# Performance work log

Hardware: AMD Instinct MI355X
Metric: run time of the kernel (lower is better)

Reference implementation:

```python
import jax, jax.numpy as jnp
import numpy as np

N_NODES = 10000
N_EDGES = 128000


def _edge_conv(x, row, col, edge_attr, w1, b1, w2, b2):
    # gather endpoints, concat edge features, 2-layer MLP per edge
    m = jnp.concatenate([x[row], x[col], edge_attr], axis=1)  # [E, 2*in+edge]
    m = jax.nn.relu(m @ w1 + b1) @ w2 + b2                    # [E, out]
    # scatter-mean onto source nodes (flow='target_to_source' -> aggregate on row)
    n = x.shape[0]
    s = jax.ops.segment_sum(m, row, num_segments=n)
    cnt = jax.ops.segment_sum(jnp.ones((row.shape[0], 1), m.dtype), row, num_segments=n)
    out = s / jnp.maximum(cnt, 1.0)
    return out, m


def setup_inputs() -> dict:
    key = jax.random.key(0)
    ks = jax.random.split(key, 24)
    f = jnp.float32

    def lin(kw, kb, fan_in, fan_out):
        lim = 1.0 / np.sqrt(fan_in)
        w = jax.random.uniform(kw, (fan_in, fan_out), f, -lim, lim)
        b = jax.random.uniform(kb, (fan_out,), f, -lim, lim)
        return w, b

    inp = {}
    inp['x_org'] = jax.random.normal(ks[0], (N_NODES, 256), f)
    inp['x_rot'] = jax.random.normal(ks[1], (N_NODES, 4), f)
    inp['edge_index'] = jax.random.randint(ks[2], (2, N_EDGES), 0, N_NODES, jnp.int64 if jax.config.jax_enable_x64 else jnp.int32)
    inp['edge_attr'] = jax.random.normal(ks[3], (N_EDGES, 640), f)
    inp['edge_rot'] = jax.random.normal(ks[4], (N_EDGES, 4), f)

    # conv1: Linear(2*260+644=1164, 64), Linear(64, 64)
    inp['c1_w1'], inp['c1_b1'] = lin(ks[5], ks[6], 1164, 64)
    inp['c1_w2'], inp['c1_b2'] = lin(ks[7], ks[8], 64, 64)
    # conv2: Linear(2*64+704=832, 64), Linear(64, 64)
    inp['c2_w1'], inp['c2_b1'] = lin(ks[9], ks[10], 832, 64)
    inp['c2_w2'], inp['c2_b2'] = lin(ks[11], ks[12], 64, 64)
    # conv3: Linear(2*128+128=384, 64), Linear(64, 64)
    inp['c3_w1'], inp['c3_b1'] = lin(ks[13], ks[14], 384, 64)
    inp['c3_w2'], inp['c3_b2'] = lin(ks[15], ks[16], 64, 64)
    # conv4: Linear(384, 64), Linear(64, 64)
    inp['c4_w1'], inp['c4_b1'] = lin(ks[17], ks[18], 384, 64)
    inp['c4_w2'], inp['c4_b2'] = lin(ks[19], ks[20], 64, 64)
    # lin1: Linear(64, 4)
    inp['lin1_w'], inp['lin1_b'] = lin(ks[21], ks[22], 64, 4)
    # edge_fc: Linear(64, 32) -> ReLU -> Linear(32, 1)
    k23 = jax.random.split(ks[23], 4)
    inp['efc_w1'], inp['efc_b1'] = lin(k23[0], k23[1], 64, 32)
    inp['efc_w2'], inp['efc_b2'] = lin(k23[2], k23[3], 32, 1)
    return inp


def reference(x_org, x_rot, edge_index, edge_attr, edge_rot,
              c1_w1, c1_b1, c1_w2, c1_b2,
              c2_w1, c2_b1, c2_w2, c2_b2,
              c3_w1, c3_b1, c3_w2, c3_b2,
              c4_w1, c4_b1, c4_w2, c4_b2,
              lin1_w, lin1_b, efc_w1, efc_b1, efc_w2, efc_b2):
    node_feat = jnp.concatenate([x_org, x_rot], axis=1)
    edge_feat = jnp.concatenate([edge_attr, edge_rot], axis=1)
    row, col = edge_index[0], edge_index[1]
    E = edge_index.shape[1]

    x1, edge_x1 = _edge_conv(node_feat, row, col, edge_feat, c1_w1, c1_b1, c1_w2, c1_b2)
    edge_x1 = jax.nn.relu(edge_x1)

    x2, edge_x2 = _edge_conv(x1, row, col, jnp.concatenate([edge_attr, edge_x1], axis=1),
                             c2_w1, c2_b1, c2_w2, c2_b2)
    x2 = jax.nn.relu(x2)
    edge_x2 = jax.nn.relu(edge_x2)

    x3, edge_x3 = _edge_conv(jnp.concatenate([x2, x1], axis=1), row, col,
                             jnp.concatenate([edge_x2, edge_x1], axis=1),
                             c3_w1, c3_b1, c3_w2, c3_b2)
    x3 = jax.nn.relu(x3)
    edge_x3 = jax.nn.relu(edge_x3)

    x4, edge_x4 = _edge_conv(jnp.concatenate([x3, x2], axis=1), row, col,
                             jnp.concatenate([edge_x3, edge_x2], axis=1),
                             c4_w1, c4_b1, c4_w2, c4_b2)
    x4 = jax.nn.relu(x4)

    x = x4 @ lin1_w + lin1_b  # [N, 4]
    h = edge_x4[: E // 2] + edge_x4[E // 2:]
    pred_edge_res = jax.nn.relu(h @ efc_w1 + efc_b1) @ efc_w2 + efc_b2  # [E/2, 1]

    # F.normalize(x, p=2, dim=1)
    x = x / jnp.maximum(jnp.linalg.norm(x, axis=1, keepdims=True), 1e-12)
    return x, pred_edge_res
```

## Files before the change

kernel.cpp:

```cpp
#include <hip/hip_runtime.h>
#include <stdint.h>


#define N_NODES 10000
#define N_EDGES 128000
#define E_HALF  64000

typedef unsigned short u16;

using bf16x8 = __attribute__((ext_vector_type(8))) short;
using f32x4  = __attribute__((ext_vector_type(4))) float;

#define MFMA16(A, B, C) C = __builtin_amdgcn_mfma_f32_16x16x32_bf16(A, B, C, 0, 0, 0)

__device__ __align__(256) float g_acc[N_NODES * 64];
__device__ __align__(256) float g_deg[N_NODES];
__device__ __align__(256) float g_P[N_NODES * 128];
__device__ __align__(256) float g_x1[N_NODES * 64];
__device__ __align__(256) float g_x2[N_NODES * 64];
__device__ __align__(256) float g_x3[N_NODES * 64];
__device__ __align__(256) float g_exA[(size_t)N_EDGES * 64];
__device__ __align__(256) float g_exB[(size_t)N_EDGES * 64];
__device__ __align__(256) u16  g_wpA_hi[11 * 4096];
__device__ __align__(256) u16  g_wpA_lo[11 * 4096];
__device__ __align__(256) u16  g_wp2_hi[4096];
__device__ __align__(256) u16  g_wp2_lo[4096];
__device__ __align__(256) u16  g_wnp_hi[4 * 8192];
__device__ __align__(256) u16  g_wnp_lo[4 * 8192];
__device__ __align__(256) int g_row[N_EDGES];
__device__ __align__(256) int g_col[N_EDGES];
__device__ int g_mode;
__device__ int g_is64;

__device__ __forceinline__ float b2f(u16 u) {
    return __uint_as_float(((unsigned int)u) << 16);
}
__device__ __forceinline__ u16 f2b(float f) {
    unsigned int u = __float_as_uint(f);
    u += 0x7FFFu + ((u >> 16) & 1u);
    return (u16)(u >> 16);
}
__device__ __forceinline__ float ldf(const u16* p)   { return b2f(*p); }
__device__ __forceinline__ float ldf(const float* p) { return *p; }
__device__ __forceinline__ void  stf(u16* p, float v)   { *p = f2b(v); }
__device__ __forceinline__ void  stf(float* p, float v) { *p = v; }

__device__ __forceinline__ float4 load4(const float* p) { return *(const float4*)p; }
__device__ __forceinline__ float4 load4(const u16* p) {
    ushort4 v = *(const ushort4*)p;
    return make_float4(b2f(v.x), b2f(v.y), b2f(v.z), b2f(v.w));
}

template<int KTB>
__device__ __forceinline__ int swz(int b) {
    return b ^ ((b >> 4) & 3) ^ (((b >> KTB) & 1) << 2);
}

__device__ __forceinline__ void split_pack(float4 v, uint2& hi, uint2& lo) {
    unsigned int ux = __float_as_uint(v.x), uy = __float_as_uint(v.y);
    unsigned int uz = __float_as_uint(v.z), uw = __float_as_uint(v.w);
    unsigned int hx = ux & 0xFFFF0000u, hy = uy & 0xFFFF0000u;
    unsigned int hz = uz & 0xFFFF0000u, hw = uw & 0xFFFF0000u;
    hi.x = (hx >> 16) | hy;
    hi.y = (hz >> 16) | hw;
    u16 lx = f2b(v.x - __uint_as_float(hx));
    u16 ly = f2b(v.y - __uint_as_float(hy));
    u16 lz = f2b(v.z - __uint_as_float(hz));
    u16 lw = f2b(v.w - __uint_as_float(hw));
    lo.x = (unsigned int)lx | ((unsigned int)ly << 16);
    lo.y = (unsigned int)lz | ((unsigned int)lw << 16);
}

__global__ void detect_kernel(const void* x_org_v, const int* __restrict__ eidx) {
    const u16* w = (const u16*)x_org_v;
    const int t = threadIdx.x;
    int ok = 0;
    for (int i = t; i < 128; i += 64) {
        u16 v = w[i];
        int ex = (v >> 7) & 0xFF;
        ok += ((ex >= 0x68 && ex <= 0x88) || ((v & 0x7FFFu) == 0)) ? 1 : 0;
    }
    #pragma unroll
    for (int off = 32; off >= 1; off >>= 1) ok += __shfl_xor(ok, off);
    bool allz = true;
    for (int i = t; i < 2048; i += 64) allz = allz && (eidx[2 * i + 1] == 0);
    unsigned long long m = __ballot(allz);
    if (t == 0) {
        g_mode = (ok >= 110) ? 0 : 1;
        g_is64 = (m == ~0ull) ? 1 : 0;
    }
}

__global__ void cvt_idx(const int* __restrict__ eidx) {
    const int e = blockIdx.x * 256 + threadIdx.x;
    if (g_is64) {
        g_row[e] = eidx[2 * e];
        g_col[e] = eidx[2 * (e + N_EDGES)];
    } else {
        g_row[e] = eidx[e];
        g_col[e] = eidx[e + N_EDGES];
    }
}

__global__ void zero_all() {
    const int i = blockIdx.x * 256 + threadIdx.x;
    g_acc[i] = 0.f;
    if (i < N_NODES) g_deg[i] = 0.f;
}

__global__ void deg_kernel() {
    const int e = blockIdx.x * 256 + threadIdx.x;
    if (e < N_EDGES) atomicAdd(&g_deg[g_row[e]], 1.0f);
}

template<typename TW>
__device__ void pack_w_body(const TW* w1, const TW* w2, int we, int ns,
                            int hioff, int nsn) {
    const int idx = blockIdx.x * 256 + threadIdx.x;
    const int t1 = ns * 4096;
    if (idx < t1) {
        const int s = idx >> 12;
        const int rem = idx & 4095;
        const int kt = rem >> 11, ct = (rem >> 9) & 3, l = (rem >> 3) & 63, r = rem & 7;
        const int k = s * 64 + kt * 32 + 4 * (l >> 4) + (r & 3) + 16 * (r >> 2);
        const float v = ldf(w1 + (size_t)(we + k) * 64 + ct * 16 + (l & 15));
        const u16 hh = f2b(v);
        g_wpA_hi[idx] = hh;
        g_wpA_lo[idx] = f2b(v - b2f(hh));
    } else if (idx < t1 + 4096) {
        const int rem = idx - t1;
        const int kt = rem >> 11, ct = (rem >> 9) & 3, l = (rem >> 3) & 63, r = rem & 7;
        const int k = kt * 32 + 4 * (l >> 4) + (r & 3) + 16 * (r >> 2);
        const float v = ldf(w2 + (size_t)k * 64 + ct * 16 + (l & 15));
        const u16 hh = f2b(v);
        g_wp2_hi[rem] = hh;
        g_wp2_lo[rem] = f2b(v - b2f(hh));
    } else if (idx < t1 + 4096 + nsn * 8192) {
        const int rem = idx - t1 - 4096;
        const int s = rem >> 13;
        const int kt = (rem >> 12) & 1, ct = (rem >> 9) & 7, l = (rem >> 3) & 63, r = rem & 7;
        const int k = s * 64 + kt * 32 + 4 * (l >> 4) + (r & 3) + 16 * (r >> 2);
        const int col = ct * 16 + (l & 15);
        const int row = (col < 64) ? k : (hioff + k);
        const float v = ldf(w1 + (size_t)row * 64 + (col & 63));
        const u16 hh = f2b(v);
        g_wnp_hi[rem] = hh;
        g_wnp_lo[rem] = f2b(v - b2f(hh));
    }
}
__global__ void pack_w_k(const void* w1, const void* w2, int we, int ns,
                         int hioff, int nsn) {
    if (g_mode == 0) pack_w_body<u16>((const u16*)w1, (const u16*)w2, we, ns, hioff, nsn);
    else             pack_w_body<float>((const float*)w1, (const float*)w2, we, ns, hioff, nsn);
}

template<typename TA, int NS1, int NS2, bool TAIL>
__device__ void node_mfma_body(u16* smA, float* smrot, float* smwt,
        const TA* A1, const float* A2, const TA* rotsrc, const TA* w1, float* P) {
    constexpr int NS = NS1 + NS2;
    const int t = threadIdx.x;
    const int lane = t & 63, wid = t >> 6;
    const int q = lane >> 4, n = lane & 15;
    const int r0b = blockIdx.x * 64;

    if constexpr (TAIL) {
        if (t < 64) {
            const int rr = min(r0b + t, N_NODES - 1);
            float4 v = load4(rotsrc + (size_t)rr * 4);
            smrot[t * 4 + 0] = v.x; smrot[t * 4 + 1] = v.y;
            smrot[t * 4 + 2] = v.z; smrot[t * 4 + 3] = v.w;
        }
        for (int i = t; i < 512; i += 256) {
            const int j = i >> 7, c = i & 127;
            const int row = (c < 64) ? (256 + j) : (516 + j);
            smwt[i] = ldf(w1 + (size_t)row * 64 + (c & 63));
        }
    }

    f32x4 acc[8];
    #pragma unroll
    for (int ct = 0; ct < 8; ++ct) acc[ct] = (f32x4){0.f, 0.f, 0.f, 0.f};

    const int eb = t >> 4;
    const int cc = t & 15;

    for (int s = 0; s < NS; ++s) {
        #pragma unroll
        for (int p = 0; p < 4; ++p) {
            const int e = p * 16 + eb;
            const int row = min(r0b + e, N_NODES - 1);
            float4 v;
            if constexpr (NS2 > 0)
                v = (s < NS1) ? load4(A1 + (size_t)row * (NS1 * 64) + s * 64 + cc * 4)
                              : load4(A2 + (size_t)row * (NS2 * 64) + (s - NS1) * 64 + cc * 4);
            else
                v = load4(A1 + (size_t)row * (NS1 * 64) + s * 64 + cc * 4);
            uint2 hi, lo; split_pack(v, hi, lo);
            const int blk = ((cc >> 3) * 4 + (e >> 4)) * 64 + (cc & 3) * 16 + (e & 15);
            const int elem = swz<8>(blk) * 8 + ((cc >> 2) & 1) * 4;
            *(uint2*)&smA[elem]        = hi;
            *(uint2*)&smA[elem + 4096] = lo;
        }
        __syncthreads();
        const u16* wph = g_wnp_hi + s * 8192;
        const u16* wpl = g_wnp_lo + s * 8192;
        #pragma unroll
        for (int kt = 0; kt < 2; ++kt) {
            const int ad = swz<8>((kt * 4 + wid) * 64 + lane) * 8;
            bf16x8 ah = *(const bf16x8*)&smA[ad];
            bf16x8 al = *(const bf16x8*)&smA[ad + 4096];
            #pragma unroll
            for (int ct = 0; ct < 8; ++ct) {
                bf16x8 bh = *(const bf16x8*)&wph[(kt * 8 + ct) * 512 + lane * 8];
                bf16x8 bl = *(const bf16x8*)&wpl[(kt * 8 + ct) * 512 + lane * 8];
                MFMA16(ah, bh, acc[ct]);
                MFMA16(al, bh, acc[ct]);
                MFMA16(ah, bl, acc[ct]);
            }
        }
        __syncthreads();
    }

    #pragma unroll
    for (int ct = 0; ct < 8; ++ct) {
        #pragma unroll
        for (int i = 0; i < 4; ++i) {
            const int rl = wid * 16 + 4 * q + i;
            const int row = r0b + rl;
            const int col = ct * 16 + n;
            float v = acc[ct][i];
            if constexpr (TAIL)
                v += smrot[rl * 4 + 0] * smwt[0 * 128 + col]
                   + smrot[rl * 4 + 1] * smwt[1 * 128 + col]
                   + smrot[rl * 4 + 2] * smwt[2 * 128 + col]
                   + smrot[rl * 4 + 3] * smwt[3 * 128 + col];
            if (row < N_NODES) P[(size_t)row * 128 + col] = v;
        }
    }
}

template<int NS1, bool TAIL>
__global__ void __launch_bounds__(256) node_mfma_in(
        const void* A1, const void* rotsrc, const void* w1, float* __restrict__ P) {
    __shared__ u16 smA[8192];
    __shared__ float smrot[256], smwt[512];
    if (g_mode == 0)
        node_mfma_body<u16, NS1, 0, TAIL>(smA, smrot, smwt, (const u16*)A1,
            nullptr, (const u16*)rotsrc, (const u16*)w1, P);
    else
        node_mfma_body<float, NS1, 0, TAIL>(smA, smrot, smwt, (const float*)A1,
            nullptr, (const float*)rotsrc, (const float*)w1, P);
}

template<int NS1, int NS2>
__global__ void __launch_bounds__(256) node_mfma_ws(
        const float* A1, const float* A2, float* __restrict__ P) {
    __shared__ u16 smA[8192];
    __shared__ float smrot[256], smwt[512];
    node_mfma_body<float, NS1, NS2, false>(smA, smrot, smwt, A1, A2,
        (const float*)nullptr, (const float*)nullptr, P);
}

template<typename TA, typename TW, int NSA, int DB, bool RELU_OUT>
__device__ __forceinline__ void edge_mfma_body(
        u16* smA, int* srow, int* scol, float* b1s, float* b2s,
        float* rot, float* wtl,
        const TA* efa, const float* efb, const TA* rotsrc,
        const TW* w1, const TW* b1v, const TW* b2v, float* eout, int we) {
    constexpr int NS_TOT = NSA + (DB == 64 ? 1 : 0);
    const int t = threadIdx.x;
    const int lane = t & 63, wid = t >> 6;
    const int q = lane >> 4, n = lane & 15;
    const int e0 = blockIdx.x * 128;

    if (t < 128) srow[t] = g_row[e0 + t];
    else         scol[t - 128] = g_col[e0 + t - 128];
    if (t >= 128 && t < 192) b1s[t - 128] = ldf(b1v + (t - 128));
    if (t >= 192)            b2s[t - 192] = ldf(b2v + (t - 192));
    if constexpr (DB == 4) {
        if (t < 128) {
            float4 r4 = load4(rotsrc + (size_t)(e0 + t) * 4);
            rot[t * 4 + 0] = r4.x; rot[t * 4 + 1] = r4.y;
            rot[t * 4 + 2] = r4.z; rot[t * 4 + 3] = r4.w;
        }
        wtl[t] = ldf(w1 + (size_t)(we + NSA * 64 + (t >> 6)) * 64 + (t & 63));
    }

    f32x4 acc[2][4];
    #pragma unroll
    for (int a_ = 0; a_ < 2; ++a_)
        #pragma unroll
        for (int b_ = 0; b_ < 4; ++b_)
            acc[a_][b_] = (f32x4){0.f, 0.f, 0.f, 0.f};

    const int eb = t >> 4;
    const int cc = t & 15;

    for (int s = 0; s < NS_TOT; ++s) {
        #pragma unroll
        for (int p = 0; p < 8; ++p) {
            const int e = p * 16 + eb;
            float4 v;
            if (s < NSA) v = load4(efa + (size_t)(e0 + e) * (NSA * 64) + s * 64 + cc * 4);
            else         v = load4(efb + (size_t)(e0 + e) * 64 + cc * 4);
            uint2 hi, lo; split_pack(v, hi, lo);
            const int blk = ((cc >> 3) * 8 + (e >> 4)) * 64 + (cc & 3) * 16 + (e & 15);
            const int elem = swz<9>(blk) * 8 + ((cc >> 2) & 1) * 4;
            *(uint2*)&smA[elem]        = hi;
            *(uint2*)&smA[elem + 8192] = lo;
        }
        __syncthreads();
        const u16* wph = g_wpA_hi + s * 4096;
        const u16* wpl = g_wpA_lo + s * 4096;
        #pragma unroll
        for (int kt = 0; kt < 2; ++kt) {
            const int b0 = (kt * 8 + wid * 2 + 0) * 64 + lane;
            const int b1 = (kt * 8 + wid * 2 + 1) * 64 + lane;
            const int r0 = swz<9>(b0) * 8;
            const int r1 = swz<9>(b1) * 8;
            bf16x8 ah0 = *(const bf16x8*)&smA[r0];
            bf16x8 ah1 = *(const bf16x8*)&smA[r1];
            bf16x8 al0 = *(const bf16x8*)&smA[r0 + 8192];
            bf16x8 al1 = *(const bf16x8*)&smA[r1 + 8192];
            #pragma unroll
            for (int ct = 0; ct < 4; ++ct) {
                bf16x8 bh = *(const bf16x8*)&wph[(kt * 4 + ct) * 512 + lane * 8];
                bf16x8 bl = *(const bf16x8*)&wpl[(kt * 4 + ct) * 512 + lane * 8];
                MFMA16(ah0, bh, acc[0][ct]);
                MFMA16(ah1, bh, acc[1][ct]);
                MFMA16(al0, bh, acc[0][ct]);
                MFMA16(al1, bh, acc[1][ct]);
                MFMA16(ah0, bl, acc[0][ct]);
                MFMA16(ah1, bl, acc[1][ct]);
            }
        }
        __syncthreads();
    }

    #pragma unroll
    for (int rt = 0; rt < 2; ++rt) {
        #pragma unroll
        for (int ct = 0; ct < 4; ++ct) {
            #pragma unroll
            for (int i = 0; i < 4; ++i) {
                const int rl = wid * 32 + rt * 16 + 4 * q + i;
                const int col = ct * 16 + n;
                float v = acc[rt][ct][i] + b1s[col]
                        + g_P[(size_t)srow[rl] * 128 + col]
                        + g_P[(size_t)scol[rl] * 128 + 64 + col];
                if constexpr (DB == 4) {
                    v += rot[rl * 4 + 0] * wtl[0 * 64 + col]
                       + rot[rl * 4 + 1] * wtl[1 * 64 + col]
                       + rot[rl * 4 + 2] * wtl[2 * 64 + col]
                       + rot[rl * 4 + 3] * wtl[3 * 64 + col];
                }
                v = fmaxf(v, 0.f);
                unsigned int hb = __float_as_uint(v) & 0xFFFF0000u;
                const u16 hh = (u16)(hb >> 16);
                const u16 hl = f2b(v - __uint_as_float(hb));
                const int off = wid * 4096
                              + (((ct >> 1) * 2 + rt) * 64 + (n >> 2) * 16 + 4 * q + i) * 8
                              + (ct & 1) * 4 + (n & 3);
                smA[off]        = hh;
                smA[off + 2048] = hl;
            }
        }
    }

    f32x4 oacc[2][4];
    #pragma unroll
    for (int rt = 0; rt < 2; ++rt)
        #pragma unroll
        for (int ct = 0; ct < 4; ++ct) {
            const float bb = b2s[ct * 16 + n];
            oacc[rt][ct] = (f32x4){bb, bb, bb, bb};
        }
    #pragma unroll
    for (int kt = 0; kt < 2; ++kt) {
        const int r0 = wid * 4096 + ((kt * 2 + 0) * 64 + lane) * 8;
        const int r1 = wid * 4096 + ((kt * 2 + 1) * 64 + lane) * 8;
        bf16x8 ah0 = *(const bf16x8*)&smA[r0];
        bf16x8 ah1 = *(const bf16x8*)&smA[r1];
        bf16x8 al0 = *(const bf16x8*)&smA[r0 + 2048];
        bf16x8 al1 = *(const bf16x8*)&smA[r1 + 2048];
        #pragma unroll
        for (int ct = 0; ct < 4; ++ct) {
            bf16x8 bh = *(const bf16x8*)&g_wp2_hi[(kt * 4 + ct) * 512 + lane * 8];
            bf16x8 bl = *(const bf16x8*)&g_wp2_lo[(kt * 4 + ct) * 512 + lane * 8];
            MFMA16(ah0, bh, oacc[0][ct]);
            MFMA16(ah1, bh, oacc[1][ct]);
            MFMA16(al0, bh, oacc[0][ct]);
            MFMA16(al1, bh, oacc[1][ct]);
            MFMA16(ah0, bl, oacc[0][ct]);
            MFMA16(ah1, bl, oacc[1][ct]);
        }
    }

    #pragma unroll
    for (int rt = 0; rt < 2; ++rt) {
        #pragma unroll
        for (int ct = 0; ct < 4; ++ct) {
            #pragma unroll
            for (int i = 0; i < 4; ++i) {
                const int rl = wid * 32 + rt * 16 + 4 * q + i;
                const int col = ct * 16 + n;
                const float v = oacc[rt][ct][i];
                atomicAdd(&g_acc[(size_t)srow[rl] * 64 + col], v);
                eout[(size_t)(e0 + rl) * 64 + col] = RELU_OUT ? fmaxf(v, 0.f) : v;
            }
        }
    }
}

template<int NSA, int DB, bool RELU_OUT>
__global__ void __launch_bounds__(256, 4) edge_mfma_in(
        const void* efa, const float* efb, const void* rotsrc,
        const void* w1, const void* b1, const void* b2, float* eout, int we) {
    __shared__ u16 smA[16384];
    __shared__ int srow[128], scol[128];
    __shared__ float b1s[64], b2s[64], rot[512], wtl[256];
    if (g_mode == 0)
        edge_mfma_body<u16, u16, NSA, DB, RELU_OUT>(smA, srow, scol, b1s, b2s, rot, wtl,
            (const u16*)efa, efb, (const u16*)rotsrc,
            (const u16*)w1, (const u16*)b1, (const u16*)b2, eout, we);
    else
        edge_mfma_body<float, float, NSA, DB, RELU_OUT>(smA, srow, scol, b1s, b2s, rot, wtl,
            (const float*)efa, efb, (const float*)rotsrc,
            (const float*)w1, (const float*)b1, (const float*)b2, eout, we);
}

template<int NSA, int DB, bool RELU_OUT>
__global__ void __launch_bounds__(256, 4) edge_mfma_ws(
        const float* efa, const float* efb,
        const void* w1, const void* b1, const void* b2, float* eout, int we) {
    __shared__ u16 smA[16384];
    __shared__ int srow[128], scol[128];
    __shared__ float b1s[64], b2s[64], rot[512], wtl[256];
    if (g_mode == 0)
        edge_mfma_body<float, u16, NSA, DB, RELU_OUT>(smA, srow, scol, b1s, b2s, rot, wtl,
            efa, efb, (const float*)nullptr,
            (const u16*)w1, (const u16*)b1, (const u16*)b2, eout, we);
    else
        edge_mfma_body<float, float, NSA, DB, RELU_OUT>(smA, srow, scol, b1s, b2s, rot, wtl,
            efa, efb, (const float*)nullptr,
            (const float*)w1, (const float*)b1, (const float*)b2, eout, we);
}

template<bool RELU>
__global__ void finalize_k(float* __restrict__ dst) {
    const int idx = blockIdx.x * 256 + threadIdx.x;
    float v = g_acc[idx] / fmaxf(g_deg[idx >> 6], 1.0f);
    g_acc[idx] = 0.f;
    if (RELU) v = fmaxf(v, 0.f);
    dst[idx] = v;
}

template<typename T>
__device__ void final_node_body(const T* w, const T* b, T* out) {
    const int t = threadIdx.x;
    const int lane = t & 63;
    const int n = blockIdx.x * 4 + (t >> 6);
    float inv = 1.0f / fmaxf(g_deg[n], 1.0f);
    float x4 = fmaxf(g_acc[(size_t)n * 64 + lane] * inv, 0.0f);
    float r[4];
    #pragma unroll
    for (int j = 0; j < 4; ++j) {
        float v = x4 * ldf(w + lane * 4 + j);
        #pragma unroll
        for (int off = 32; off >= 1; off >>= 1) v += __shfl_xor(v, off);
        r[j] = v + ldf(b + j);
    }
    float nrm = sqrtf(r[0]*r[0] + r[1]*r[1] + r[2]*r[2] + r[3]*r[3]);
    float dn = fmaxf(nrm, 1e-12f);
    if (lane < 4) stf(out + n * 4 + lane, r[lane] / dn);
}
__global__ void final_node(const void* w, const void* b, void* out) {
    if (g_mode == 0) final_node_body<u16>((const u16*)w, (const u16*)b, (u16*)out);
    else             final_node_body<float>((const float*)w, (const float*)b, (float*)out);
}

template<typename T>
__device__ void edge_head_body(const float* ex4, const T* w1, const T* b1,
                               const T* w2, const T* b2, T* out) {
    __shared__ float lw1[2048];
    __shared__ float lw2[32];
    const int t = threadIdx.x;
    for (int i = t; i < 2048; i += 256) lw1[i] = ldf(w1 + i);
    if (t < 32) lw2[t] = ldf(w2 + t);
    __syncthreads();
    const int e = blockIdx.x * 256 + t;
    float a[32];
    #pragma unroll
    for (int j = 0; j < 32; ++j) a[j] = ldf(b1 + j);
    const float* p0 = ex4 + (size_t)e * 64;
    const float* p1 = ex4 + (size_t)(e + E_HALF) * 64;
    for (int c = 0; c < 64; ++c) {
        float h = p0[c] + p1[c];
        #pragma unroll
        for (int j = 0; j < 32; ++j) a[j] += h * lw1[c * 32 + j];
    }
    float s = ldf(b2);
    #pragma unroll
    for (int j = 0; j < 32; ++j) s += fmaxf(a[j], 0.f) * lw2[j];
    stf(out + e, s);
}
__global__ void __launch_bounds__(256) edge_head(const float* ex4,
        const void* w1, const void* b1, const void* w2, const void* b2,
        void* out) {
    if (g_mode == 0)
        edge_head_body<u16>(ex4, (const u16*)w1, (const u16*)b1,
                            (const u16*)w2, (const u16*)b2, (u16*)out + 40000);
    else
        edge_head_body<float>(ex4, (const float*)w1, (const float*)b1,
                              (const float*)w2, (const float*)b2, (float*)out + 40000);
}

__global__ void sentinel_fill(unsigned int* out, int n_words) {
    int i = blockIdx.x * 256 + threadIdx.x;
    if (i < n_words) out[i] = 0x44794479u;
}

static void* sym_addr(const void* symbol) {
    void* p = nullptr;
    (void)hipGetSymbolAddress(&p, symbol);
    return p;
}

extern "C" void kernel_launch(void* const* d_in, const int* in_sizes, int n_in,
                              void* d_out, int out_size, void* d_ws, size_t ws_size,
                              hipStream_t stream) {
    (void)d_ws; (void)ws_size;
    bool ok = (n_in == 27) && (out_size == 104000)
           && (in_sizes[0] == 2560000) && (in_sizes[2] == 256000)
           && (in_sizes[3] == 81920000) && (in_sizes[5] == 74496)
           && (in_sizes[21] == 256) && (in_sizes[25] == 32);
    if (!ok) {
        sentinel_fill<<<204, 256, 0, stream>>>((unsigned int*)d_out, 52000);
        return;
    }
    const void* x_org     = d_in[0];
    const void* x_rot     = d_in[1];
    const int*  eidx      = (const int*)d_in[2];
    const void* edge_attr = d_in[3];
    const void* edge_rot  = d_in[4];

    float* P   = (float*)sym_addr(HIP_SYMBOL(g_P));
    float* x1  = (float*)sym_addr(HIP_SYMBOL(g_x1));
    float* x2  = (float*)sym_addr(HIP_SYMBOL(g_x2));
    float* x3  = (float*)sym_addr(HIP_SYMBOL(g_x3));
    float* exA = (float*)sym_addr(HIP_SYMBOL(g_exA));
    float* exB = (float*)sym_addr(HIP_SYMBOL(g_exB));

    detect_kernel<<<1, 64, 0, stream>>>(x_org, eidx);
    cvt_idx<<<500, 256, 0, stream>>>(eidx);
    zero_all<<<2500, 256, 0, stream>>>();
    deg_kernel<<<500, 256, 0, stream>>>();

    pack_w_k<<<304, 256, 0, stream>>>(d_in[5], d_in[7], 520, 10, 260, 4);
    node_mfma_in<4, true><<<157, 256, 0, stream>>>(x_org, x_rot, d_in[5], P);
    edge_mfma_in<10, 4, true><<<1000, 256, 0, stream>>>(
        edge_attr, nullptr, edge_rot, d_in[5], d_in[6], d_in[8], exA, 520);
    finalize_k<false><<<2500, 256, 0, stream>>>(x1);

    pack_w_k<<<224, 256, 0, stream>>>(d_in[9], d_in[11], 128, 11, 64, 1);
    node_mfma_ws<1, 0><<<157, 256, 0, stream>>>(x1, nullptr, P);
    edge_mfma_in<10, 64, true><<<1000, 256, 0, stream>>>(
        edge_attr, exA, nullptr, d_in[9], d_in[10], d_in[12], exB, 128);
    finalize_k<true><<<2500, 256, 0, stream>>>(x2);

    pack_w_k<<<112, 256, 0, stream>>>(d_in[13], d_in[15], 256, 2, 128, 2);
    node_mfma_ws<1, 1><<<157, 256, 0, stream>>>(x2, x1, P);
    edge_mfma_ws<1, 64, true><<<1000, 256, 0, stream>>>(
        exB, exA, d_in[13], d_in[14], d_in[16], exA, 256);
    finalize_k<true><<<2500, 256, 0, stream>>>(x3);

    pack_w_k<<<112, 256, 0, stream>>>(d_in[17], d_in[19], 256, 2, 128, 2);
    node_mfma_ws<1, 1><<<157, 256, 0, stream>>>(x3, x2, P);
    edge_mfma_ws<1, 64, false><<<1000, 256, 0, stream>>>(
        exA, exB, d_in[17], d_in[18], d_in[20], exB, 256);

    final_node<<<2500, 256, 0, stream>>>(d_in[21], d_in[22], d_out);
    edge_head<<<250, 256, 0, stream>>>(exB, d_in[23], d_in[24], d_in[25], d_in[26],
                                       d_out);
}
```

Baseline: 922.8 us.

## Fuse edge_attr projections for conv1/conv2 and pass edge features as MFMA fragments

The conv1 edge kernel now multiplies edge_attr by a combined 128-column weight holding both the conv1 and conv2 edge_attr rows. The conv2 contribution is saved to a Q2 buffer, so conv2 no longer re-reads the 640-wide edge_attr. Intermediate edge outputs are written as pre-split bf16 hi/lo MFMA fragment tiles, and later layers load them straight into registers instead of repacking fp32 through shared memory. This removes a second full pass over the large edge_attr tensor and the repacking cost. In exchange it adds a Q2 round trip and more accumulator registers in conv1, with occupancy lowered to 3 blocks per unit.

```diff
diff --git a/kernel.cpp b/kernel.cpp
--- a/kernel.cpp
+++ b/kernel.cpp
@@ -5,6 +5,7 @@
 #define N_NODES 10000
 #define N_EDGES 128000
 #define E_HALF  64000
+#define NBLK    1000
 
 typedef unsigned short u16;
 
@@ -19,14 +20,18 @@
 __device__ __align__(256) float g_x1[N_NODES * 64];
 __device__ __align__(256) float g_x2[N_NODES * 64];
 __device__ __align__(256) float g_x3[N_NODES * 64];
-__device__ __align__(256) float g_exA[(size_t)N_EDGES * 64];
-__device__ __align__(256) float g_exB[(size_t)N_EDGES * 64];
-__device__ __align__(256) u16  g_wpA_hi[11 * 4096];
-__device__ __align__(256) u16  g_wpA_lo[11 * 4096];
+__device__ __align__(256) u16  g_fragA[(size_t)NBLK * 16384];
+__device__ __align__(256) u16  g_fragB[(size_t)NBLK * 16384];
+__device__ __align__(256) float g_Q2 [(size_t)N_EDGES * 64];
+__device__ __align__(256) float g_ex4[(size_t)N_EDGES * 64];
+__device__ __align__(256) u16  g_wpA_hi[2 * 4096];
+__device__ __align__(256) u16  g_wpA_lo[2 * 4096];
 __device__ __align__(256) u16  g_wp2_hi[4096];
 __device__ __align__(256) u16  g_wp2_lo[4096];
 __device__ __align__(256) u16  g_wnp_hi[4 * 8192];
 __device__ __align__(256) u16  g_wnp_lo[4 * 8192];
+__device__ __align__(256) u16  g_wpC_hi[10 * 8192];
+__device__ __align__(256) u16  g_wpC_lo[10 * 8192];
 __device__ __align__(256) int g_row[N_EDGES];
 __device__ __align__(256) int g_col[N_EDGES];
 __device__ int g_mode;
@@ -114,20 +119,22 @@
 }
 
 template<typename TW>
-__device__ void pack_w_body(const TW* w1, const TW* w2, int we, int ns,
-                            int hioff, int nsn) {
+__device__ void pack_w_body(const TW* w1a, const TW* w2, const TW* w1b,
+                            int we, int ns, int hioff, int nsn, int nsc) {
     const int idx = blockIdx.x * 256 + threadIdx.x;
     const int t1 = ns * 4096;
+    const int t2 = t1 + 4096;
+    const int t3 = t2 + nsn * 8192;
     if (idx < t1) {
         const int s = idx >> 12;
         const int rem = idx & 4095;
         const int kt = rem >> 11, ct = (rem >> 9) & 3, l = (rem >> 3) & 63, r = rem & 7;
         const int k = s * 64 + kt * 32 + 4 * (l >> 4) + (r & 3) + 16 * (r >> 2);
-        const float v = ldf(w1 + (size_t)(we + k) * 64 + ct * 16 + (l & 15));
+        const float v = ldf(w1a + (size_t)(we + k) * 64 + ct * 16 + (l & 15));
         const u16 hh = f2b(v);
         g_wpA_hi[idx] = hh;
         g_wpA_lo[idx] = f2b(v - b2f(hh));
-    } else if (idx < t1 + 4096) {
+    } else if (idx < t2) {
         const int rem = idx - t1;
         const int kt = rem >> 11, ct = (rem >> 9) & 3, l = (rem >> 3) & 63, r = rem & 7;
         const int k = kt * 32 + 4 * (l >> 4) + (r & 3) + 16 * (r >> 2);
@@ -135,23 +142,39 @@
         const u16 hh = f2b(v);
         g_wp2_hi[rem] = hh;
         g_wp2_lo[rem] = f2b(v - b2f(hh));
-    } else if (idx < t1 + 4096 + nsn * 8192) {
-        const int rem = idx - t1 - 4096;
+    } else if (idx < t3) {
+        const int rem = idx - t2;
         const int s = rem >> 13;
         const int kt = (rem >> 12) & 1, ct = (rem >> 9) & 7, l = (rem >> 3) & 63, r = rem & 7;
         const int k = s * 64 + kt * 32 + 4 * (l >> 4) + (r & 3) + 16 * (r >> 2);
         const int col = ct * 16 + (l & 15);
         const int row = (col < 64) ? k : (hioff + k);
-        const float v = ldf(w1 + (size_t)row * 64 + (col & 63));
+        const float v = ldf(w1a + (size_t)row * 64 + (col & 63));
         const u16 hh = f2b(v);
         g_wnp_hi[rem] = hh;
         g_wnp_lo[rem] = f2b(v - b2f(hh));
-    }
-}
-__global__ void pack_w_k(const void* w1, const void* w2, int we, int ns,
-                         int hioff, int nsn) {
-    if (g_mode == 0) pack_w_body<u16>((const u16*)w1, (const u16*)w2, we, ns, hioff, nsn);
-    else             pack_w_body<float>((const float*)w1, (const float*)w2, we, ns, hioff, nsn);
+    } else if (idx < t3 + nsc * 8192) {
+        const int rem = idx - t3;
+        const int s = rem >> 13;
+        const int kt = (rem >> 12) & 1, ct = (rem >> 9) & 7, l = (rem >> 3) & 63, r = rem & 7;
+        const int k = s * 64 + kt * 32 + 4 * (l >> 4) + (r & 3) + 16 * (r >> 2);
+        const int col = ct * 16 + (l & 15);
+        float v;
+        if (col < 64) v = ldf(w1a + (size_t)(520 + k) * 64 + col);
+        else          v = ldf(w1b + (size_t)(128 + k) * 64 + (col - 64));
+        const u16 hh = f2b(v);
+        g_wpC_hi[rem] = hh;
+        g_wpC_lo[rem] = f2b(v - b2f(hh));
+    }
+}
+__global__ void pack_w_k(const void* w1a, const void* w2, const void* w1b,
+                         int we, int ns, int hioff, int nsn, int nsc) {
+    if (g_mode == 0)
+        pack_w_body<u16>((const u16*)w1a, (const u16*)w2, (const u16*)w1b,
+                         we, ns, hioff, nsn, nsc);
+    else
+        pack_w_body<float>((const float*)w1a, (const float*)w2, (const float*)w1b,
+                         we, ns, hioff, nsn, nsc);
 }
 
 template<typename TA, int NS1, int NS2, bool TAIL>
@@ -261,13 +284,44 @@
         (const float*)nullptr, (const float*)nullptr, P);
 }
 
-template<typename TA, typename TW, int NSA, int DB, bool RELU_OUT>
-__device__ __forceinline__ void edge_mfma_body(
-        u16* smA, int* srow, int* scol, float* b1s, float* b2s,
-        float* rot, float* wtl,
-        const TA* efa, const float* efb, const TA* rotsrc,
-        const TW* w1, const TW* b1v, const TW* b2v, float* eout, int we) {
-    constexpr int NS_TOT = NSA + (DB == 64 ? 1 : 0);
+__device__ __forceinline__ void frag_store_o(u16* smA, int wid, int lane,
+        const f32x4 (&oacc)[2][4], u16* Fdst, int blkid) {
+    const int q = lane >> 4, n = lane & 15;
+    #pragma unroll
+    for (int rt = 0; rt < 2; ++rt)
+        #pragma unroll
+        for (int ct = 0; ct < 4; ++ct)
+            #pragma unroll
+            for (int i = 0; i < 4; ++i) {
+                float v = fmaxf(oacc[rt][ct][i], 0.f);
+                unsigned int hb = __float_as_uint(v) & 0xFFFF0000u;
+                const u16 hh = (u16)(hb >> 16);
+                const u16 hl = f2b(v - __uint_as_float(hb));
+                const int off = wid * 4096
+                              + (((ct >> 1) * 2 + rt) * 64 + (n >> 2) * 16 + 4 * q + i) * 8
+                              + (ct & 1) * 4 + (n & 3);
+                smA[off]        = hh;
+                smA[off + 2048] = hl;
+            }
+    #pragma unroll
+    for (int kt = 0; kt < 2; ++kt)
+        #pragma unroll
+        for (int rtl = 0; rtl < 2; ++rtl) {
+            const int src = wid * 4096 + ((kt * 2 + rtl) * 64 + lane) * 8;
+            bf16x8 h8 = *(const bf16x8*)&smA[src];
+            bf16x8 l8 = *(const bf16x8*)&smA[src + 2048];
+            const size_t gb = (size_t)blkid * 16384
+                            + (size_t)(kt * 8 + wid * 2 + rtl) * 512 + lane * 8;
+            *(bf16x8*)&Fdst[gb]        = h8;
+            *(bf16x8*)&Fdst[gb + 8192] = l8;
+        }
+}
+
+template<typename TA, typename TW>
+__device__ void edge_c1_body(u16* smA, int* srow, int* scol,
+        float* b1s, float* b2s, float* rot, float* wtl,
+        const TA* efa, const TA* rotsrc,
+        const TW* w1, const TW* b1v, const TW* b2v) {
     const int t = threadIdx.x;
     const int lane = t & 63, wid = t >> 6;
     const int q = lane >> 4, n = lane & 15;
@@ -277,32 +331,28 @@
     else         scol[t - 128] = g_col[e0 + t - 128];
     if (t >= 128 && t < 192) b1s[t - 128] = ldf(b1v + (t - 128));
     if (t >= 192)            b2s[t - 192] = ldf(b2v + (t - 192));
-    if constexpr (DB == 4) {
-        if (t < 128) {
-            float4 r4 = load4(rotsrc + (size_t)(e0 + t) * 4);
-            rot[t * 4 + 0] = r4.x; rot[t * 4 + 1] = r4.y;
-            rot[t * 4 + 2] = r4.z; rot[t * 4 + 3] = r4.w;
-        }
-        wtl[t] = ldf(w1 + (size_t)(we + NSA * 64 + (t >> 6)) * 64 + (t & 63));
-    }
-
-    f32x4 acc[2][4];
+    if (t < 128) {
+        float4 r4 = load4(rotsrc + (size_t)(e0 + t) * 4);
+        rot[t * 4 + 0] = r4.x; rot[t * 4 + 1] = r4.y;
+        rot[t * 4 + 2] = r4.z; rot[t * 4 + 3] = r4.w;
+    }
+    wtl[t] = ldf(w1 + (size_t)(1160 + (t >> 6)) * 64 + (t & 63));
+
+    f32x4 acc[2][8];
     #pragma unroll
     for (int a_ = 0; a_ < 2; ++a_)
         #pragma unroll
-        for (int b_ = 0; b_ < 4; ++b_)
+        for (int b_ = 0; b_ < 8; ++b_)
             acc[a_][b_] = (f32x4){0.f, 0.f, 0.f, 0.f};
 
     const int eb = t >> 4;
     const int cc = t & 15;
 
-    for (int s = 0; s < NS_TOT; ++s) {
+    for (int s = 0; s < 10; ++s) {
         #pragma unroll
         for (int p = 0; p < 8; ++p) {
             const int e = p * 16 + eb;
-            float4 v;
-            if (s < NSA) v = load4(efa + (size_t)(e0 + e) * (NSA * 64) + s * 64 + cc * 4);
-            else         v = load4(efb + (size_t)(e0 + e) * 64 + cc * 4);
+            float4 v = load4(efa + (size_t)(e0 + e) * 640 + s * 64 + cc * 4);
             uint2 hi, lo; split_pack(v, hi, lo);
             const int blk = ((cc >> 3) * 8 + (e >> 4)) * 64 + (cc & 3) * 16 + (e & 15);
             const int elem = swz<9>(blk) * 8 + ((cc >> 2) & 1) * 4;
@@ -310,18 +360,163 @@
             *(uint2*)&smA[elem + 8192] = lo;
         }
         __syncthreads();
-        const u16* wph = g_wpA_hi + s * 4096;
-        const u16* wpl = g_wpA_lo + s * 4096;
+        const u16* wph = g_wpC_hi + s * 8192;
+        const u16* wpl = g_wpC_lo + s * 8192;
         #pragma unroll
         for (int kt = 0; kt < 2; ++kt) {
             const int b0 = (kt * 8 + wid * 2 + 0) * 64 + lane;
-            const int b1 = (kt * 8 + wid * 2 + 1) * 64 + lane;
+            const int b1i = (kt * 8 + wid * 2 + 1) * 64 + lane;
             const int r0 = swz<9>(b0) * 8;
-            const int r1 = swz<9>(b1) * 8;
+            const int r1 = swz<9>(b1i) * 8;
             bf16x8 ah0 = *(const bf16x8*)&smA[r0];
             bf16x8 ah1 = *(const bf16x8*)&smA[r1];
             bf16x8 al0 = *(const bf16x8*)&smA[r0 + 8192];
             bf16x8 al1 = *(const bf16x8*)&smA[r1 + 8192];
+            #pragma unroll
+            for (int ct = 0; ct < 8; ++ct) {
+                bf16x8 bh = *(const bf16x8*)&wph[(kt * 8 + ct) * 512 + lane * 8];
+                bf16x8 bl = *(const bf16x8*)&wpl[(kt * 8 + ct) * 512 + lane * 8];
+                MFMA16(ah0, bh, acc[0][ct]);
+                MFMA16(ah1, bh, acc[1][ct]);
+                MFMA16(al0, bh, acc[0][ct]);
+                MFMA16(al1, bh, acc[1][ct]);
+                MFMA16(ah0, bl, acc[0][ct]);
+                MFMA16(ah1, bl, acc[1][ct]);
+            }
+        }
+        __syncthreads();
+    }
+
+    #pragma unroll
+    for (int rt = 0; rt < 2; ++rt)
+        #pragma unroll
+        for (int c2 = 0; c2 < 4; ++c2)
+            #pragma unroll
+            for (int i = 0; i < 4; ++i) {
+                const int rl = wid * 32 + rt * 16 + 4 * q + i;
+                g_Q2[(size_t)(e0 + rl) * 64 + c2 * 16 + n] = acc[rt][4 + c2][i];
+            }
+
+    #pragma unroll
+    for (int rt = 0; rt < 2; ++rt)
+        #pragma unroll
+        for (int ct = 0; ct < 4; ++ct)
+            #pragma unroll
+            for (int i = 0; i < 4; ++i) {
+                const int rl = wid * 32 + rt * 16 + 4 * q + i;
+                const int col = ct * 16 + n;
+                float v = acc[rt][ct][i] + b1s[col]
+                        + g_P[(size_t)srow[rl] * 128 + col]
+                        + g_P[(size_t)scol[rl] * 128 + 64 + col]
+                        + rot[rl * 4 + 0] * wtl[0 * 64 + col]
+                        + rot[rl * 4 + 1] * wtl[1 * 64 + col]
+                        + rot[rl * 4 + 2] * wtl[2 * 64 + col]
+                        + rot[rl * 4 + 3] * wtl[3 * 64 + col];
+                v = fmaxf(v, 0.f);
+                unsigned int hb = __float_as_uint(v) & 0xFFFF0000u;
+                const u16 hh = (u16)(hb >> 16);
+                const u16 hl = f2b(v - __uint_as_float(hb));
+                const int off = wid * 4096
+                              + (((ct >> 1) * 2 + rt) * 64 + (n >> 2) * 16 + 4 * q + i) * 8
+                              + (ct & 1) * 4 + (n & 3);
+                smA[off]        = hh;
+                smA[off + 2048] = hl;
+            }
+
+    f32x4 oacc[2][4];
+    #pragma unroll
+    for (int rt = 0; rt < 2; ++rt)
+        #pragma unroll
+        for (int ct = 0; ct < 4; ++ct) {
+            const float bb = b2s[ct * 16 + n];
+            oacc[rt][ct] = (f32x4){bb, bb, bb, bb};
+        }
+    #pragma unroll
+    for (int kt = 0; kt < 2; ++kt) {
+        const int r0 = wid * 4096 + ((kt * 2 + 0) * 64 + lane) * 8;
+        const int r1 = wid * 4096 + ((kt * 2 + 1) * 64 + lane) * 8;
+        bf16x8 ah0 = *(const bf16x8*)&smA[r0];
+        bf16x8 ah1 = *(const bf16x8*)&smA[r1];
+        bf16x8 al0 = *(const bf16x8*)&smA[r0 + 2048];
+        bf16x8 al1 = *(const bf16x8*)&smA[r1 + 2048];
+        #pragma unroll
+        for (int ct = 0; ct < 4; ++ct) {
+            bf16x8 bh = *(const bf16x8*)&g_wp2_hi[(kt * 4 + ct) * 512 + lane * 8];
+            bf16x8 bl = *(const bf16x8*)&g_wp2_lo[(kt * 4 + ct) * 512 + lane * 8];
+            MFMA16(ah0, bh, oacc[0][ct]);
+            MFMA16(ah1, bh, oacc[1][ct]);
+            MFMA16(al0, bh, oacc[0][ct]);
+            MFMA16(al1, bh, oacc[1][ct]);
+            MFMA16(ah0, bl, oacc[0][ct]);
+            MFMA16(ah1, bl, oacc[1][ct]);
+        }
+    }
+
+    #pragma unroll
+    for (int rt = 0; rt < 2; ++rt)
+        #pragma unroll
+        for (int ct = 0; ct < 4; ++ct)
+            #pragma unroll
+            for (int i = 0; i < 4; ++i) {
+                const int rl = wid * 32 + rt * 16 + 4 * q + i;
+                atomicAdd(&g_acc[(size_t)srow[rl] * 64 + ct * 16 + n], oacc[rt][ct][i]);
+            }
+    frag_store_o(smA, wid, lane, oacc, g_fragA, blockIdx.x);
+}
+
+__global__ void __launch_bounds__(256, 3) edge_c1(
+        const void* efa, const void* rotsrc,
+        const void* w1, const void* b1, const void* b2) {
+    __shared__ u16 smA[16384];
+    __shared__ int srow[128], scol[128];
+    __shared__ float b1s[64], b2s[64], rot[512], wtl[256];
+    if (g_mode == 0)
+        edge_c1_body<u16, u16>(smA, srow, scol, b1s, b2s, rot, wtl,
+            (const u16*)efa, (const u16*)rotsrc,
+            (const u16*)w1, (const u16*)b1, (const u16*)b2);
+    else
+        edge_c1_body<float, float>(smA, srow, scol, b1s, b2s, rot, wtl,
+            (const float*)efa, (const float*)rotsrc,
+            (const float*)w1, (const float*)b1, (const float*)b2);
+}
+
+template<typename TW, int NSF, bool HASQ2, bool FRAG_OUT>
+__device__ void edge_lite_body(u16* smA, int* srow, int* scol,
+        float* b1s, float* b2s,
+        const u16* f0, const u16* f1,
+        const TW* b1v, const TW* b2v, u16* Ffrag, float* fout) {
+    const int t = threadIdx.x;
+    const int lane = t & 63, wid = t >> 6;
+    const int q = lane >> 4, n = lane & 15;
+    const int e0 = blockIdx.x * 128;
+    const size_t blkb = (size_t)blockIdx.x * 16384;
+
+    if (t < 128) srow[t] = g_row[e0 + t];
+    else         scol[t - 128] = g_col[e0 + t - 128];
+    if (t >= 128 && t < 192) b1s[t - 128] = ldf(b1v + (t - 128));
+    if (t >= 192)            b2s[t - 192] = ldf(b2v + (t - 192));
+    __syncthreads();
+
+    f32x4 acc[2][4];
+    #pragma unroll
+    for (int a_ = 0; a_ < 2; ++a_)
+        #pragma unroll
+        for (int b_ = 0; b_ < 4; ++b_)
+            acc[a_][b_] = (f32x4){0.f, 0.f, 0.f, 0.f};
+
+    #pragma unroll
+    for (int s = 0; s < NSF; ++s) {
+        const u16* fs = (s == 0) ? f0 : f1;
+        const u16* wph = g_wpA_hi + s * 4096;
+        const u16* wpl = g_wpA_lo + s * 4096;
+        #pragma unroll
+        for (int kt = 0; kt < 2; ++kt) {
+            const size_t ba0 = blkb + (size_t)(kt * 8 + wid * 2 + 0) * 512 + lane * 8;
+            const size_t ba1 = blkb + (size_t)(kt * 8 + wid * 2 + 1) * 512 + lane * 8;
+            bf16x8 ah0 = *(const bf16x8*)&fs[ba0];
+            bf16x8 al0 = *(const bf16x8*)&fs[ba0 + 8192];
+            bf16x8 ah1 = *(const bf16x8*)&fs[ba1];
+            bf16x8 al1 = *(const bf16x8*)&fs[ba1 + 8192];
             #pragma unroll
             for (int ct = 0; ct < 4; ++ct) {
                 bf16x8 bh = *(const bf16x8*)&wph[(kt * 4 + ct) * 512 + lane * 8];
@@ -334,13 +529,12 @@
                 MFMA16(ah1, bl, acc[1][ct]);
             }
         }
-        __syncthreads();
-    }
-
-    #pragma unroll
-    for (int rt = 0; rt < 2; ++rt) {
-        #pragma unroll
-        for (int ct = 0; ct < 4; ++ct) {
+    }
+
+    #pragma unroll
+    for (int rt = 0; rt < 2; ++rt)
+        #pragma unroll
+        for (int ct = 0; ct < 4; ++ct)
             #pragma unroll
             for (int i = 0; i < 4; ++i) {
                 const int rl = wid * 32 + rt * 16 + 4 * q + i;
@@ -348,12 +542,8 @@
                 float v = acc[rt][ct][i] + b1s[col]
                         + g_P[(size_t)srow[rl] * 128 + col]
                         + g_P[(size_t)scol[rl] * 128 + 64 + col];
-                if constexpr (DB == 4) {
-                    v += rot[rl * 4 + 0] * wtl[0 * 64 + col]
-                       + rot[rl * 4 + 1] * wtl[1 * 64 + col]
-                       + rot[rl * 4 + 2] * wtl[2 * 64 + col]
-                       + rot[rl * 4 + 3] * wtl[3 * 64 + col];
-                }
+                if constexpr (HASQ2)
+                    v += g_Q2[(size_t)(e0 + rl) * 64 + col];
                 v = fmaxf(v, 0.f);
                 unsigned int hb = __float_as_uint(v) & 0xFFFF0000u;
                 const u16 hh = (u16)(hb >> 16);
@@ -364,8 +554,6 @@
                 smA[off]        = hh;
                 smA[off + 2048] = hl;
             }
-        }
-    }
 
     f32x4 oacc[2][4];
     #pragma unroll
@@ -397,53 +585,35 @@
     }
 
     #pragma unroll
-    for (int rt = 0; rt < 2; ++rt) {
-        #pragma unroll
-        for (int ct = 0; ct < 4; ++ct) {
+    for (int rt = 0; rt < 2; ++rt)
+        #pragma unroll
+        for (int ct = 0; ct < 4; ++ct)
             #pragma unroll
             for (int i = 0; i < 4; ++i) {
                 const int rl = wid * 32 + rt * 16 + 4 * q + i;
                 const int col = ct * 16 + n;
                 const float v = oacc[rt][ct][i];
                 atomicAdd(&g_acc[(size_t)srow[rl] * 64 + col], v);
-                eout[(size_t)(e0 + rl) * 64 + col] = RELU_OUT ? fmaxf(v, 0.f) : v;
-            }
-        }
-    }
-}
-
-template<int NSA, int DB, bool RELU_OUT>
-__global__ void __launch_bounds__(256, 4) edge_mfma_in(
-        const void* efa, const float* efb, const void* rotsrc,
-        const void* w1, const void* b1, const void* b2, float* eout, int we) {
+                if constexpr (!FRAG_OUT)
+                    fout[(size_t)(e0 + rl) * 64 + col] = v;
+            }
+    if constexpr (FRAG_OUT)
+        frag_store_o(smA, wid, lane, oacc, Ffrag, blockIdx.x);
+}
+
+template<int NSF, bool HASQ2, bool FRAG_OUT>
+__global__ void __launch_bounds__(256, 4) edge_lite(
+        const u16* f0, const u16* f1, const void* b1, const void* b2,
+        u16* Ffrag, float* fout) {
     __shared__ u16 smA[16384];
     __shared__ int srow[128], scol[128];
-    __shared__ float b1s[64], b2s[64], rot[512], wtl[256];
+    __shared__ float b1s[64], b2s[64];
     if (g_mode == 0)
-        edge_mfma_body<u16, u16, NSA, DB, RELU_OUT>(smA, srow, scol, b1s, b2s, rot, wtl,
-            (const u16*)efa, efb, (const u16*)rotsrc,
-            (const u16*)w1, (const u16*)b1, (const u16*)b2, eout, we);
+        edge_lite_body<u16, NSF, HASQ2, FRAG_OUT>(smA, srow, scol, b1s, b2s,
+            f0, f1, (const u16*)b1, (const u16*)b2, Ffrag, fout);
     else
-        edge_mfma_body<float, float, NSA, DB, RELU_OUT>(smA, srow, scol, b1s, b2s, rot, wtl,
-            (const float*)efa, efb, (const float*)rotsrc,
-            (const float*)w1, (const float*)b1, (const float*)b2, eout, we);
-}
-
-template<int NSA, int DB, bool RELU_OUT>
-__global__ void __launch_bounds__(256, 4) edge_mfma_ws(
-        const float* efa, const float* efb,
-        const void* w1, const void* b1, const void* b2, float* eout, int we) {
-    __shared__ u16 smA[16384];
-    __shared__ int srow[128], scol[128];
-    __shared__ float b1s[64], b2s[64], rot[512], wtl[256];
-    if (g_mode == 0)
-        edge_mfma_body<float, u16, NSA, DB, RELU_OUT>(smA, srow, scol, b1s, b2s, rot, wtl,
-            efa, efb, (const float*)nullptr,
-            (const u16*)w1, (const u16*)b1, (const u16*)b2, eout, we);
-    else
-        edge_mfma_body<float, float, NSA, DB, RELU_OUT>(smA, srow, scol, b1s, b2s, rot, wtl,
-            efa, efb, (const float*)nullptr,
-            (const float*)w1, (const float*)b1, (const float*)b2, eout, we);
+        edge_lite_body<float, NSF, HASQ2, FRAG_OUT>(smA, srow, scol, b1s, b2s,
+            f0, f1, (const float*)b1, (const float*)b2, Ffrag, fout);
 }
 
 template<bool RELU>
@@ -548,38 +718,38 @@
     float* x1  = (float*)sym_addr(HIP_SYMBOL(g_x1));
     float* x2  = (float*)sym_addr(HIP_SYMBOL(g_x2));
     float* x3  = (float*)sym_addr(HIP_SYMBOL(g_x3));
-    float* exA = (float*)sym_addr(HIP_SYMBOL(g_exA));
-    float* exB = (float*)sym_addr(HIP_SYMBOL(g_exB));
+    u16*   fA  = (u16*)sym_addr(HIP_SYMBOL(g_fragA));
+    u16*   fB  = (u16*)sym_addr(HIP_SYMBOL(g_fragB));
+    float* ex4 = (float*)sym_addr(HIP_SYMBOL(g_ex4));
 
     detect_kernel<<<1, 64, 0, stream>>>(x_org, eidx);
     cvt_idx<<<500, 256, 0, stream>>>(eidx);
     zero_all<<<2500, 256, 0, stream>>>();
     deg_kernel<<<500, 256, 0, stream>>>();
 
-    pack_w_k<<<304, 256, 0, stream>>>(d_in[5], d_in[7], 520, 10, 260, 4);
+    pack_w_k<<<464, 256, 0, stream>>>(d_in[5], d_in[7], d_in[9], 0, 0, 260, 4, 10);
     node_mfma_in<4, true><<<157, 256, 0, stream>>>(x_org, x_rot, d_in[5], P);
-    edge_mfma_in<10, 4, true><<<1000, 256, 0, stream>>>(
-        edge_attr, nullptr, edge_rot, d_in[5], d_in[6], d_in[8], exA, 520);
+    edge_c1<<<NBLK, 256, 0, stream>>>(edge_attr, edge_rot, d_in[5], d_in[6], d_in[8]);
     finalize_k<false><<<2500, 256, 0, stream>>>(x1);
 
-    pack_w_k<<<224, 256, 0, stream>>>(d_in[9], d_in[11], 128, 11, 64, 1);
+    pack_w_k<<<64, 256, 0, stream>>>(d_in[9], d_in[11], d_in[9], 768, 1, 64, 1, 0);
     node_mfma_ws<1, 0><<<157, 256, 0, stream>>>(x1, nullptr, P);
-    edge_mfma_in<10, 64, true><<<1000, 256, 0, stream>>>(
-        edge_attr, exA, nullptr, d_in[9], d_in[10], d_in[12], exB, 128);
+    edge_lite<1, true, true><<<NBLK, 256, 0, stream>>>(
+        fA, nullptr, d_in[10], d_in[12], fB, nullptr);
     finalize_k<true><<<2500, 256, 0, stream>>>(x2);
 
-    pack_w_k<<<112, 256, 0, stream>>>(d_in[13], d_in[15], 256, 2, 128, 2);
+    pack_w_k<<<112, 256, 0, stream>>>(d_in[13], d_in[15], d_in[13], 256, 2, 128, 2, 0);
     node_mfma_ws<1, 1><<<157, 256, 0, stream>>>(x2, x1, P);
-    edge_mfma_ws<1, 64, true><<<1000, 256, 0, stream>>>(
-        exB, exA, d_in[13], d_in[14], d_in[16], exA, 256);
+    edge_lite<2, false, true><<<NBLK, 256, 0, stream>>>(
+        fB, fA, d_in[14], d_in[16], fA, nullptr);
     finalize_k<true><<<2500, 256, 0, stream>>>(x3);
 
-    pack_w_k<<<112, 256, 0, stream>>>(d_in[17], d_in[19], 256, 2, 128, 2);
+    pack_w_k<<<112, 256, 0, stream>>>(d_in[17], d_in[19], d_in[17], 256, 2, 128, 2, 0);
     node_mfma_ws<1, 1><<<157, 256, 0, stream>>>(x3, x2, P);
-    edge_mfma_ws<1, 64, false><<<1000, 256, 0, stream>>>(
-        exA, exB, d_in[17], d_in[18], d_in[20], exB, 256);
+    edge_lite<2, false, false><<<NBLK, 256, 0, stream>>>(
+        fA, fB, d_in[18], d_in[20], nullptr, ex4);
 
     final_node<<<2500, 256, 0, stream>>>(d_in[21], d_in[22], d_out);
-    edge_head<<<250, 256, 0, stream>>>(exB, d_in[23], d_in[24], d_in[25], d_in[26],
+    edge_head<<<250, 256, 0, stream>>>(ex4, d_in[23], d_in[24], d_in[25], d_in[26],
                                        d_out);
 }
```

Result: slower. 943.1 us (+2.2%).
